# Kernel optimization log

Measured on AMD Instinct MI355X. Metric: run time of the kernel, lower is better.

## Reference

```python
import jax, jax.numpy as jnp
import numpy as np

# static architecture constants (match init_kwargs)
H, D, N_BASIS, MEM_LEN, QLEN = 16, 128, 1024, 512, 2048
RIDGE = 0.5
BASIS_SIGMAS = (0.005, 0.01)


def _gaussian_pdf(x, mu, sigma):
    return jnp.exp(-0.5 * ((x - mu) / sigma) ** 2) / (sigma * jnp.sqrt(2.0 * jnp.pi))


def _basis_params(n):
    # torch.meshgrid(linspace(0,1,n//2), sigmas, indexing='ij') then flatten
    m = jnp.linspace(0.0, 1.0, n // len(BASIS_SIGMAS)).astype(jnp.float32)
    mu = jnp.repeat(m, len(BASIS_SIGMAS))
    sigma = jnp.tile(jnp.asarray(BASIS_SIGMAS, jnp.float32), n // len(BASIS_SIGMAS))
    return mu, sigma


def _compute_G(l, b_mu, b_sigma, n):
    # padded linear positions on [-0.5+shift, 1.5-shift], l even -> 2l points
    shift = 1.0 / (2 * l)
    pos = jnp.linspace(-0.5 + shift, 1.5 - shift, 2 * l).astype(jnp.float32)
    F = _gaussian_pdf(pos[None, :], b_mu[:, None], b_sigma[:, None])  # [N, 2l]
    # G = F^T (F F^T + ridge I)^{-1}, then crop padding rows -> [l, N]
    G = jnp.linalg.solve(F @ F.T + RIDGE * jnp.eye(n, dtype=jnp.float32), F).T
    return G[l // 2: -(l // 2)]


def _forward(k, q, W_key, W_val, W_out, w_mu, w_sigma):
    d = H * D
    b_mu, b_sigma = _basis_params(N_BASIS)
    k = k[:, -512:, :]                                   # forward truncates memory
    l = k.shape[1]
    G = _compute_G(l, b_mu, b_sigma, N_BASIS)            # [l, N]
    # value_function: project signal onto basis coefficients B -> [1, N, d]
    B = jnp.einsum('bld,ln->bnd', k, G)
    keys = (B @ W_key.T).reshape(1, N_BASIS, H, D).transpose(0, 2, 1, 3)    # [1,H,N,D]
    values = (B @ W_val.T).reshape(1, N_BASIS, H, D).transpose(0, 2, 1, 3)  # [1,H,N,D]
    scores = jnp.einsum('bhqd,bhnd->bhqn', q / jnp.sqrt(jnp.float32(D)), keys)
    mu = jax.nn.sigmoid(scores @ w_mu)[..., None]                           # [1,H,Q,1]
    sigma_sq = jnp.maximum(jax.nn.softplus(scores @ w_sigma), 1e-4)[..., None]
    # continuous softmax over Gaussian RBFs: r_j = E_{t~N(mu,sigma_sq)}[psi_j(t)]
    # closed form: N(mu; b_mu_j, sigma_sq + b_sigma_j^2)
    r = _gaussian_pdf(b_mu, mu, jnp.sqrt(sigma_sq + b_sigma ** 2))          # [1,H,Q,N]
    context = jnp.einsum('bhqn,bhnd->bqhd', r, values).reshape(1, QLEN, d)
    return context @ W_out.T


def setup_inputs() -> dict:
    key = jax.random.key(0)
    ks = jax.random.split(key, 7)
    d = H * D
    s = 0.02
    return {
        'k': jax.random.normal(ks[0], (1, MEM_LEN, d), jnp.float32),
        'q': jax.random.normal(ks[1], (1, H, QLEN, D), jnp.float32),
        'W_key': jax.random.normal(ks[2], (d, d), jnp.float32) * s,
        'W_val': jax.random.normal(ks[3], (d, d), jnp.float32) * s,
        'W_out': jax.random.normal(ks[4], (d, d), jnp.float32) * s,
        'w_mu': jax.random.normal(ks[5], (N_BASIS,), jnp.float32) * s,
        'w_sigma': jax.random.normal(ks[6], (N_BASIS,), jnp.float32) * s,
        'new_doc': 1,
    }


def reference(k, q, W_key, W_val, W_out, w_mu, w_sigma, new_doc):
    # new_doc=True -> B_past/x_past reset, so only the fresh-memory path runs
    return _forward(k, q, W_key, W_val, W_out, w_mu, w_sigma)
```

## Files before the change

### kernel.cpp

```cpp
#include <hip/hip_runtime.h>
#include <hip/hip_bf16.h>
#include <vector>
#include <cmath>
#include <cstring>

using bf16 = __hip_bfloat16;
typedef short s16x8 __attribute__((ext_vector_type(8)));
typedef float f32x4 __attribute__((ext_vector_type(4)));

static constexpr int kH = 16, kD = 128, kNB = 1024, kML = 512, kQL = 2048, kDM = 2048;

static void compute_Gt_host(float* Gt) {
  const int n = kNB, P = 2 * kML;
  std::vector<double> F((size_t)n * P), A((size_t)n * n), pos(P);
  const double shift = 1.0 / (double)P;
  const double p0 = -0.5 + shift, p1 = 1.5 - shift;
  for (int i = 0; i < P; i++) pos[i] = p0 + (p1 - p0) * (double)i / (double)(P - 1);
  const double c0 = 0.3989422804014327;
  std::vector<int> lo(n), hi(n);
  for (int b = 0; b < n; b++) {
    double mu = (double)(b >> 1) / 511.0;
    double sg = (b & 1) ? 0.01 : 0.005;
    double c = c0 / sg;
    double* Fb = &F[(size_t)b * P];
    for (int i = 0; i < P; i++) { double t = (pos[i] - mu) / sg; Fb[i] = c * exp(-0.5 * t * t); }
    int l = 0; while (l < P - 1 && pos[l] < mu - 14.0 * sg) l++;
    int h = P - 1; while (h > 0 && pos[h] > mu + 14.0 * sg) h--;
    lo[b] = l; hi[b] = h;
  }
  for (int i = 0; i < n; i++) {
    const double* fi = &F[(size_t)i * P];
    for (int j = 0; j <= i; j++) {
      const double* fj = &F[(size_t)j * P];
      int a = lo[i] > lo[j] ? lo[i] : lo[j];
      int b2 = hi[i] < hi[j] ? hi[i] : hi[j];
      double s = 0.0;
      for (int k2 = a; k2 <= b2; k2++) s += fi[k2] * fj[k2];
      A[(size_t)i * n + j] = s;
      if (i != j) A[(size_t)j * n + i] = s;
    }
    A[(size_t)i * n + i] += 0.5;
  }
  for (int j = 0; j < n; j++) {
    double* Aj = &A[(size_t)j * n];
    double d = Aj[j];
    for (int k2 = 0; k2 < j; k2++) d -= Aj[k2] * Aj[k2];
    d = std::sqrt(d); Aj[j] = d;
    double inv = 1.0 / d;
    for (int i = j + 1; i < n; i++) {
      double* Ai = &A[(size_t)i * n];
      double s = Ai[j];
      for (int k2 = 0; k2 < j; k2++) s -= Ai[k2] * Aj[k2];
      Ai[j] = s * inv;
    }
  }
  for (int i = 0; i < n; i++) {
    double* yi = &F[(size_t)i * P];
    const double* Ai = &A[(size_t)i * n];
    for (int k2 = 0; k2 < i; k2++) {
      double lik = Ai[k2];
      const double* yk = &F[(size_t)k2 * P];
      for (int t = 0; t < P; t++) yi[t] -= lik * yk[t];
    }
    double inv = 1.0 / Ai[i];
    for (int t = 0; t < P; t++) yi[t] *= inv;
  }
  for (int i = n - 1; i >= 0; i--) {
    double* xi = &F[(size_t)i * P];
    for (int k2 = i + 1; k2 < n; k2++) {
      double lki = A[(size_t)k2 * n + i];
      const double* xk = &F[(size_t)k2 * P];
      for (int t = 0; t < P; t++) xi[t] -= lki * xk[t];
    }
    double inv = 1.0 / A[(size_t)i * n + i];
    for (int t = 0; t < P; t++) xi[t] *= inv;
  }
  for (int b = 0; b < n; b++)
    for (int l = 0; l < kML; l++)
      Gt[(size_t)b * kML + l] = (float)F[(size_t)b * P + (kML / 2) + l];
}

static unsigned short f2bf_host(float x) {
  unsigned u; std::memcpy(&u, &x, 4);
  unsigned r = (u + 0x7FFFu + ((u >> 16) & 1u)) >> 16;
  return (unsigned short)r;
}
static float bf2f_host(unsigned short b) {
  unsigned u = ((unsigned)b) << 16; float f; std::memcpy(&f, &u, 4); return f;
}

namespace {
struct Init {
  float* d_GtTf = nullptr;
  unsigned short* d_Gth = nullptr;
  unsigned short* d_Gtl = nullptr;
  float* h_GtTf_pinned = nullptr;
  unsigned short* h_Gth_pinned = nullptr;
  unsigned short* h_Gtl_pinned = nullptr;
  std::vector<float> h_GtTf;
  std::vector<unsigned short> h_Gth, h_Gtl;
  Init() {
    std::vector<float> h_Gt((size_t)kNB * kML);
    compute_Gt_host(h_Gt.data());
    h_GtTf.resize(h_Gt.size());
    h_Gth.resize(h_Gt.size());
    h_Gtl.resize(h_Gt.size());
    for (int n = 0; n < kNB; n++)
      for (int l = 0; l < kML; l++) {
        float v = h_Gt[(size_t)n * kML + l];
        h_GtTf[(size_t)l * kNB + n] = v;
        unsigned short hb = f2bf_host(v);
        h_Gth[(size_t)n * kML + l] = hb;
        h_Gtl[(size_t)n * kML + l] = f2bf_host(v - bf2f_host(hb));
      }
    const size_t fb = h_Gt.size() * 4, bb = h_Gt.size() * 2;
    if (hipMalloc((void**)&d_GtTf, fb) == hipSuccess) {
      if (hipMemcpy(d_GtTf, h_GtTf.data(), fb, hipMemcpyHostToDevice) != hipSuccess) { hipFree(d_GtTf); d_GtTf = nullptr; }
    }
    if (hipMalloc((void**)&d_Gth, bb) == hipSuccess) {
      if (hipMemcpy(d_Gth, h_Gth.data(), bb, hipMemcpyHostToDevice) != hipSuccess) { hipFree(d_Gth); d_Gth = nullptr; }
    }
    if (hipMalloc((void**)&d_Gtl, bb) == hipSuccess) {
      if (hipMemcpy(d_Gtl, h_Gtl.data(), bb, hipMemcpyHostToDevice) != hipSuccess) { hipFree(d_Gtl); d_Gtl = nullptr; }
    }
    if (!d_GtTf && hipHostMalloc((void**)&h_GtTf_pinned, fb, 0) == hipSuccess)
      std::memcpy(h_GtTf_pinned, h_GtTf.data(), fb);
    if (!d_Gth && hipHostMalloc((void**)&h_Gth_pinned, bb, 0) == hipSuccess)
      std::memcpy(h_Gth_pinned, h_Gth.data(), bb);
    if (!d_Gtl && hipHostMalloc((void**)&h_Gtl_pinned, bb, 0) == hipSuccess)
      std::memcpy(h_Gtl_pinned, h_Gtl.data(), bb);
  }
};
Init g_init;
}

__device__ inline short f2bf(float x) {
  unsigned u = __float_as_uint(x);
  unsigned r = (u + 0x7FFFu + ((u >> 16) & 1u)) >> 16;
  return (short)r;
}
__device__ inline float bf2f(short b) {
  return __uint_as_float(((unsigned)(unsigned short)b) << 16);
}

__global__ __launch_bounds__(256) void detect_kernel(const unsigned short* __restrict__ q,
                                                     int* __restrict__ flag) {
  int t = threadIdx.x;
  int bad = 0;
  for (int i = t; i < 4096; i += 256) {
    int e = (q[i] >> 7) & 0xFF;
    if (e >= 0x98) bad = 1;
  }
  __shared__ int s[256];
  s[t] = bad; __syncthreads();
  for (int k2 = 128; k2 > 0; k2 >>= 1) { if (t < k2) s[t] |= s[t + k2]; __syncthreads(); }
  if (t == 0) *flag = s[0];
}

__global__ __launch_bounds__(256) void conv_bf16(const void* __restrict__ in,
                                                 short* __restrict__ out, int n4,
                                                 const int* __restrict__ flag) {
  int i = blockIdx.x * 256 + threadIdx.x;
  if (i >= n4) return;
  if (*flag) {
    float4 v = ((const float4*)in)[i];
    short4 o; o.x = f2bf(v.x); o.y = f2bf(v.y); o.z = f2bf(v.z); o.w = f2bf(v.w);
    ((short4*)out)[i] = o;
  } else {
    ((short4*)out)[i] = ((const short4*)in)[i];
  }
}

__global__ __launch_bounds__(256) void gw_kernel(const float* __restrict__ GtT,
                                                 const void* __restrict__ wmu,
                                                 const void* __restrict__ wsg,
                                                 float* __restrict__ gw,
                                                 const int* __restrict__ flag) {
  const bool f32 = (*flag != 0);
  const int l = blockIdx.x, t = threadIdx.x;
  const float* row = GtT + (long long)l * kNB;
  float a = 0.f, b = 0.f;
  for (int n = t; n < kNB; n += 256) {
    float g = row[n];
    float wm_ = f32 ? ((const float*)wmu)[n] : bf2f(((const short*)wmu)[n]);
    float ws_ = f32 ? ((const float*)wsg)[n] : bf2f(((const short*)wsg)[n]);
    a += g * wm_; b += g * ws_;
  }
  __shared__ float red[2][256];
  red[0][t] = a; red[1][t] = b;
  __syncthreads();
  for (int s = 128; s > 0; s >>= 1) {
    if (t < s) { red[0][t] += red[0][t + s]; red[1][t] += red[1][t + s]; }
    __syncthreads();
  }
  if (t == 0) { gw[l] = red[0][0]; gw[kML + l] = red[1][0]; }
}

__global__ __launch_bounds__(256) void bwk_kernel(const void* __restrict__ kin,
                                                  const float* __restrict__ gw,
                                                  float* __restrict__ bw,
                                                  const int* __restrict__ flag) {
  const bool f32 = (*flag != 0);
  int j = blockIdx.x * 256 + threadIdx.x;
  int l0 = blockIdx.y * 32;
  float a = 0.f, b = 0.f;
  for (int l = l0; l < l0 + 32; l++) {
    float kv = f32 ? ((const float*)kin)[(long long)l * kDM + j]
                   : bf2f(((const short*)kin)[(long long)l * kDM + j]);
    a += kv * gw[l]; b += kv * gw[kML + l];
  }
  atomicAdd(&bw[j], a);
  atomicAdd(&bw[kDM + j], b);
}

__global__ __launch_bounds__(256) void kw_kernel(const void* __restrict__ Wk,
                                                 const float* __restrict__ bw,
                                                 float* __restrict__ kw,
                                                 const int* __restrict__ flag) {
  const bool f32 = (*flag != 0);
  int i = blockIdx.x;
  float smu = 0.f, ssg = 0.f;
  if (f32) {
    const float* row = (const float*)Wk + (long long)i * kDM;
    for (int j = threadIdx.x; j < kDM; j += 256) { float w = row[j]; smu += w * bw[j]; ssg += w * bw[kDM + j]; }
  } else {
    const short* row = (const short*)Wk + (long long)i * kDM;
    for (int j = threadIdx.x; j < kDM; j += 256) { float w = bf2f(row[j]); smu += w * bw[j]; ssg += w * bw[kDM + j]; }
  }
  __shared__ float red[2][256];
  red[0][threadIdx.x] = smu; red[1][threadIdx.x] = ssg;
  __syncthreads();
  for (int s = 128; s > 0; s >>= 1) {
    if (threadIdx.x < (unsigned)s) {
      red[0][threadIdx.x] += red[0][threadIdx.x + s];
      red[1][threadIdx.x] += red[1][threadIdx.x + s];
    }
    __syncthreads();
  }
  if (threadIdx.x == 0) { kw[i] = red[0][0]; kw[kDM + i] = red[1][0]; }
}

__global__ __launch_bounds__(256) void musig_kernel(const void* __restrict__ q,
                                                    const float* __restrict__ kw,
                                                    float* __restrict__ mu,
                                                    float* __restrict__ sigsq,
                                                    const int* __restrict__ flag) {
  const bool f32 = (*flag != 0);
  int w = threadIdx.x >> 6, lane = threadIdx.x & 63;
  int idx = blockIdx.x * 4 + w;
  int h = idx >> 11;
  const float* kmu = kw + h * kD;
  const float* ksg = kw + kDM + h * kD;
  float q0, q1;
  if (f32) {
    const float* qrow = (const float*)q + (long long)idx * kD;
    q0 = qrow[lane]; q1 = qrow[lane + 64];
  } else {
    const short* qrow = (const short*)q + (long long)idx * kD;
    q0 = bf2f(qrow[lane]); q1 = bf2f(qrow[lane + 64]);
  }
  float a = q0 * kmu[lane] + q1 * kmu[lane + 64];
  float b = q0 * ksg[lane] + q1 * ksg[lane + 64];
  for (int s = 32; s > 0; s >>= 1) { a += __shfl_xor(a, s); b += __shfl_xor(b, s); }
  if (lane == 0) {
    const float inv_sqrt_d = 0.08838834764831845f;
    float zm = a * inv_sqrt_d, zs = b * inv_sqrt_d;
    mu[idx] = 1.f / (1.f + __expf(-zm));
    float sp = (zs > 20.f) ? zs : log1pf(__expf(zs));
    sigsq[idx] = fmaxf(sp, 1e-4f);
  }
}

template <int CSTORE>
__global__ __launch_bounds__(256) void mfma_gemm_bt(
    const short* __restrict__ A0, int lda, long long sA,
    const short* __restrict__ BT0, int ldb, long long sB,
    void* __restrict__ C0, int ldc, long long sC,
    int K, const int* __restrict__ flag) {
  __shared__ s16x8 lA[512];
  __shared__ s16x8 lB[512];
  const short* A = A0 + (long long)blockIdx.z * sA;
  const short* BT = BT0 + (long long)blockIdx.z * sB;
  const int t = threadIdx.x;
  const int wave = t >> 6, lane = t & 63;
  const int quad = lane >> 4, l16 = lane & 15;
  const int wm = wave >> 1, wn = wave & 1;
  const int m0 = blockIdx.y * 128, n0 = blockIdx.x * 128;
  const int r0 = t >> 2, kc = t & 3;
  f32x4 acc[4][4];
  const f32x4 z = {0.f, 0.f, 0.f, 0.f};
#pragma unroll
  for (int i = 0; i < 4; i++)
#pragma unroll
    for (int j = 0; j < 4; j++) acc[i][j] = z;
  for (int k0 = 0; k0 < K; k0 += 32) {
#pragma unroll
    for (int i = 0; i < 2; i++) {
      int m = r0 + i * 64;
      int cidx = (m >> 4) * 64 + kc * 16 + (m & 15);
      lA[cidx] = *(const s16x8*)(A + (long long)(m0 + m) * lda + k0 + kc * 8);
      lB[cidx] = *(const s16x8*)(BT + (long long)(n0 + m) * ldb + k0 + kc * 8);
    }
    __syncthreads();
    s16x8 af[4], bfr[4];
#pragma unroll
    for (int i = 0; i < 4; i++) af[i] = lA[(wm * 4 + i) * 64 + lane];
#pragma unroll
    for (int j = 0; j < 4; j++) bfr[j] = lB[(wn * 4 + j) * 64 + lane];
#pragma unroll
    for (int i = 0; i < 4; i++)
#pragma unroll
      for (int j = 0; j < 4; j++)
        acc[i][j] = __builtin_amdgcn_mfma_f32_16x16x32_bf16(af[i], bfr[j], acc[i][j], 0, 0, 0);
    __syncthreads();
  }
  if (CSTORE == 0) {
    short* Cp = (short*)C0 + (long long)blockIdx.z * sC;
#pragma unroll
    for (int i = 0; i < 4; i++)
#pragma unroll
      for (int j = 0; j < 4; j++) {
        int gn = n0 + (wn * 4 + j) * 16 + l16;
#pragma unroll
        for (int rg = 0; rg < 4; rg++) {
          int gm = m0 + (wm * 4 + i) * 16 + quad * 4 + rg;
          Cp[(long long)gm * ldc + gn] = f2bf(acc[i][j][rg]);
        }
      }
  } else if (CSTORE == 1) {
    short* Cp = (short*)C0 + (long long)blockIdx.z * sC;
#pragma unroll
    for (int i = 0; i < 4; i++)
#pragma unroll
      for (int j = 0; j < 4; j++) {
        int gn = n0 + (wn * 4 + j) * 16 + l16;
        int gm = m0 + (wm * 4 + i) * 16 + quad * 4;
        short4 p; p.x = f2bf(acc[i][j][0]); p.y = f2bf(acc[i][j][1]);
        p.z = f2bf(acc[i][j][2]); p.w = f2bf(acc[i][j][3]);
        *(short4*)(Cp + (long long)gn * ldc + gm) = p;
      }
  } else {
    if (*flag) {
      float* Cp = (float*)C0 + (long long)blockIdx.z * sC;
#pragma unroll
      for (int i = 0; i < 4; i++)
#pragma unroll
        for (int j = 0; j < 4; j++) {
          int gn = n0 + (wn * 4 + j) * 16 + l16;
#pragma unroll
          for (int rg = 0; rg < 4; rg++) {
            int gm = m0 + (wm * 4 + i) * 16 + quad * 4 + rg;
            Cp[(long long)gm * ldc + gn] = acc[i][j][rg];
          }
        }
    } else {
      short* Cp = (short*)C0 + (long long)blockIdx.z * sC;
#pragma unroll
      for (int i = 0; i < 4; i++)
#pragma unroll
        for (int j = 0; j < 4; j++) {
          int gn = n0 + (wn * 4 + j) * 16 + l16;
#pragma unroll
          for (int rg = 0; rg < 4; rg++) {
            int gm = m0 + (wm * 4 + i) * 16 + quad * 4 + rg;
            Cp[(long long)gm * ldc + gn] = f2bf(acc[i][j][rg]);
          }
        }
    }
  }
}

__global__ __launch_bounds__(256) void mfma_gemm_bt2(
    const short* __restrict__ A0, int lda,
    const short* __restrict__ BTh, const short* __restrict__ BTl, int ldb,
    short* __restrict__ Ch, short* __restrict__ Cl, int ldc, int K) {
  __shared__ s16x8 lA[512], lBh[512], lBl[512];
  const int t = threadIdx.x;
  const int wave = t >> 6, lane = t & 63;
  const int quad = lane >> 4, l16 = lane & 15;
  const int wm = wave >> 1, wn = wave & 1;
  const int m0 = blockIdx.y * 128, n0 = blockIdx.x * 128;
  const int r0 = t >> 2, kc = t & 3;
  f32x4 acc[4][4];
  const f32x4 z = {0.f, 0.f, 0.f, 0.f};
#pragma unroll
  for (int i = 0; i < 4; i++)
#pragma unroll
    for (int j = 0; j < 4; j++) acc[i][j] = z;
  for (int k0 = 0; k0 < K; k0 += 32) {
#pragma unroll
    for (int i = 0; i < 2; i++) {
      int m = r0 + i * 64;
      int cidx = (m >> 4) * 64 + kc * 16 + (m & 15);
      lA[cidx]  = *(const s16x8*)(A0 + (long long)(m0 + m) * lda + k0 + kc * 8);
      lBh[cidx] = *(const s16x8*)(BTh + (long long)(n0 + m) * ldb + k0 + kc * 8);
      lBl[cidx] = *(const s16x8*)(BTl + (long long)(n0 + m) * ldb + k0 + kc * 8);
    }
    __syncthreads();
    s16x8 af[4], bh[4], bl[4];
#pragma unroll
    for (int i = 0; i < 4; i++) af[i] = lA[(wm * 4 + i) * 64 + lane];
#pragma unroll
    for (int j = 0; j < 4; j++) {
      bh[j] = lBh[(wn * 4 + j) * 64 + lane];
      bl[j] = lBl[(wn * 4 + j) * 64 + lane];
    }
#pragma unroll
    for (int i = 0; i < 4; i++)
#pragma unroll
      for (int j = 0; j < 4; j++) {
        acc[i][j] = __builtin_amdgcn_mfma_f32_16x16x32_bf16(af[i], bh[j], acc[i][j], 0, 0, 0);
        acc[i][j] = __builtin_amdgcn_mfma_f32_16x16x32_bf16(af[i], bl[j], acc[i][j], 0, 0, 0);
      }
    __syncthreads();
  }
#pragma unroll
  for (int i = 0; i < 4; i++)
#pragma unroll
    for (int j = 0; j < 4; j++) {
      int gn = n0 + (wn * 4 + j) * 16 + l16;
#pragma unroll
      for (int rg = 0; rg < 4; rg++) {
        int gm = m0 + (wm * 4 + i) * 16 + quad * 4 + rg;
        float v = acc[i][j][rg];
        short hb = f2bf(v);
        Ch[(long long)gm * ldc + gn] = hb;
        Cl[(long long)gm * ldc + gn] = f2bf(v - bf2f(hb));
      }
    }
}

__global__ __launch_bounds__(256) void mfma_rv(
    const float* __restrict__ mu_all, const float* __restrict__ s2_all,
    const short* __restrict__ VTh, const short* __restrict__ VTl,
    short* __restrict__ ctx) {
  __shared__ s16x8 lAh[512], lAl[512], lBh[512], lBl[512];
  const int t = threadIdx.x;
  const int wave = t >> 6, lane = t & 63;
  const int quad = lane >> 4, l16 = lane & 15;
  const int wm = wave >> 1, wn = wave & 1;
  const int h = blockIdx.z;
  const int m0 = blockIdx.y * 128;
  const int r0 = t >> 2, kc = t & 3;
  const long long voff = (long long)h * kD * kNB;
  float muv[2], ivs[2][2], cof[2][2];
#pragma unroll
  for (int i = 0; i < 2; i++) {
    int row = h * kQL + m0 + r0 + i * 64;
    float m_ = mu_all[row], s2 = s2_all[row];
    ivs[i][0] = rsqrtf(s2 + 2.5e-5f);
    ivs[i][1] = rsqrtf(s2 + 1e-4f);
    cof[i][0] = 0.3989422804014327f * ivs[i][0];
    cof[i][1] = 0.3989422804014327f * ivs[i][1];
    muv[i] = m_;
  }
  f32x4 acc[4][4];
  const f32x4 z = {0.f, 0.f, 0.f, 0.f};
#pragma unroll
  for (int i = 0; i < 4; i++)
#pragma unroll
    for (int j = 0; j < 4; j++) acc[i][j] = z;
  for (int k0 = 0; k0 < kNB; k0 += 32) {
#pragma unroll
    for (int i = 0; i < 2; i++) {
      int m = r0 + i * 64;
      int cidx = (m >> 4) * 64 + kc * 16 + (m & 15);
      s16x8 hv, lv;
#pragma unroll
      for (int jj = 0; jj < 8; jj++) {
        int n = k0 + kc * 8 + jj;
        float bmu = (float)(n >> 1) * (1.f / 511.f);
        int p = jj & 1;
        float tt = (bmu - muv[i]) * ivs[i][p];
        float v = cof[i][p] * __expf(-0.5f * tt * tt);
        short hb = f2bf(v);
        hv[jj] = hb;
        lv[jj] = f2bf(v - bf2f(hb));
      }
      lAh[cidx] = hv;
      lAl[cidx] = lv;
      lBh[cidx] = *(const s16x8*)(VTh + voff + (long long)m * kNB + k0 + kc * 8);
      lBl[cidx] = *(const s16x8*)(VTl + voff + (long long)m * kNB + k0 + kc * 8);
    }
    __syncthreads();
    s16x8 ah[4], al[4], bh[4], bl[4];
#pragma unroll
    for (int i = 0; i < 4; i++) {
      ah[i] = lAh[(wm * 4 + i) * 64 + lane];
      al[i] = lAl[(wm * 4 + i) * 64 + lane];
    }
#pragma unroll
    for (int j = 0; j < 4; j++) {
      bh[j] = lBh[(wn * 4 + j) * 64 + lane];
      bl[j] = lBl[(wn * 4 + j) * 64 + lane];
    }
#pragma unroll
    for (int i = 0; i < 4; i++)
#pragma unroll
      for (int j = 0; j < 4; j++) {
        acc[i][j] = __builtin_amdgcn_mfma_f32_16x16x32_bf16(ah[i], bh[j], acc[i][j], 0, 0, 0);
        acc[i][j] = __builtin_amdgcn_mfma_f32_16x16x32_bf16(ah[i], bl[j], acc[i][j], 0, 0, 0);
        acc[i][j] = __builtin_amdgcn_mfma_f32_16x16x32_bf16(al[i], bh[j], acc[i][j], 0, 0, 0);
      }
    __syncthreads();
  }
  short* Cp = ctx + h * kD;
#pragma unroll
  for (int i = 0; i < 4; i++)
#pragma unroll
    for (int j = 0; j < 4; j++) {
      int gn = (wn * 4 + j) * 16 + l16;
#pragma unroll
      for (int rg = 0; rg < 4; rg++) {
        int gm = m0 + (wm * 4 + i) * 16 + quad * 4 + rg;
        Cp[(long long)gm * kDM + gn] = f2bf(acc[i][j][rg]);
      }
    }
}

extern "C" void kernel_launch(void* const* d_in, const int* in_sizes, int n_in,
                              void* d_out, int out_size, void* d_ws, size_t ws_size,
                              hipStream_t stream) {
  (void)in_sizes; (void)n_in; (void)out_size; (void)ws_size;
  const void* kmem = d_in[0];
  const void* q    = d_in[1];
  const void* Wk   = d_in[2];
  const void* Wv   = d_in[3];
  const void* Wo   = d_in[4];
  const void* wmu  = d_in[5];
  const void* wsg  = d_in[6];

  char* ws = (char*)d_ws;
  short* k_bf  = (short*)ws;
  short* kvT   = (short*)(ws + ((size_t)2 << 20));
  short* Wv_bf = (short*)(ws + ((size_t)4 << 20));
  short* Wo_bf = Wv_bf;
  short* VTh   = (short*)(ws + ((size_t)12 << 20));
  short* VTl   = (short*)(ws + ((size_t)16 << 20));
  short* ctx   = (short*)(ws + ((size_t)20 << 20));
  float* tail  = (float*)(ws + ((size_t)28 << 20));
  float* gw    = tail;
  float* bw    = gw + 2 * kML;
  float* kw    = bw + 2 * kDM;
  float* mu    = kw + 2 * kDM;
  float* sigsq = mu + kH * kQL;
  int*   flag  = (int*)(sigsq + kH * kQL);
  float* gtffall = (float*)(ws + ((size_t)28 << 20) + ((size_t)1 << 19));
  short* ghfall  = (short*)(ws + ((size_t)30 << 20) + ((size_t)1 << 19));
  short* glfall  = (short*)(ws + ((size_t)31 << 20) + ((size_t)1 << 19));

  const float* GtTf = g_init.d_GtTf;
  if (!GtTf) {
    const void* src = g_init.h_GtTf_pinned ? (const void*)g_init.h_GtTf_pinned
                                           : (const void*)g_init.h_GtTf.data();
    hipMemcpyAsync(gtffall, src, (size_t)kNB * kML * 4, hipMemcpyHostToDevice, stream);
    GtTf = gtffall;
  }
  const short* Gh = (const short*)g_init.d_Gth;
  if (!Gh) {
    const void* src = g_init.h_Gth_pinned ? (const void*)g_init.h_Gth_pinned
                                          : (const void*)g_init.h_Gth.data();
    hipMemcpyAsync(ghfall, src, (size_t)kNB * kML * 2, hipMemcpyHostToDevice, stream);
    Gh = ghfall;
  }
  const short* Gl = (const short*)g_init.d_Gtl;
  if (!Gl) {
    const void* src = g_init.h_Gtl_pinned ? (const void*)g_init.h_Gtl_pinned
                                          : (const void*)g_init.h_Gtl.data();
    hipMemcpyAsync(glfall, src, (size_t)kNB * kML * 2, hipMemcpyHostToDevice, stream);
    Gl = glfall;
  }

  detect_kernel<<<1, 256, 0, stream>>>((const unsigned short*)q, flag);

  conv_bf16<<<(kML * kDM / 4 + 255) / 256, 256, 0, stream>>>(kmem, k_bf, kML * kDM / 4, flag);
  conv_bf16<<<(kDM * kDM / 4 + 255) / 256, 256, 0, stream>>>(Wv, Wv_bf, kDM * kDM / 4, flag);

  gw_kernel<<<kML, 256, 0, stream>>>(GtTf, wmu, wsg, gw, flag);
  hipMemsetAsync(bw, 0, 2 * kDM * sizeof(float), stream);
  bwk_kernel<<<dim3(kDM / 256, kML / 32), 256, 0, stream>>>(kmem, gw, bw, flag);
  kw_kernel<<<kDM, 256, 0, stream>>>(Wk, bw, kw, flag);
  musig_kernel<<<kH * kQL / 4, 256, 0, stream>>>(q, kw, mu, sigsq, flag);

  mfma_gemm_bt<1><<<dim3(kDM / 128, kML / 128, 1), 256, 0, stream>>>(
      k_bf, kDM, 0, Wv_bf, kDM, 0, kvT, kML, 0, kDM, flag);

  conv_bf16<<<(kDM * kDM / 4 + 255) / 256, 256, 0, stream>>>(Wo, Wo_bf, kDM * kDM / 4, flag);

  mfma_gemm_bt2<<<dim3(kNB / 128, kDM / 128, 1), 256, 0, stream>>>(
      kvT, kML, Gh, Gl, kML, VTh, VTl, kNB, kML);

  mfma_rv<<<dim3(1, kQL / 128, kH), 256, 0, stream>>>(mu, sigsq, VTh, VTl, ctx);

  mfma_gemm_bt<2><<<dim3(kDM / 128, kQL / 128, 1), 256, 0, stream>>>(
      ctx, kDM, 0, Wo_bf, kDM, 0, d_out, kDM, 0, kDM, flag);
}
```

Measured before the change: 320.9 us.

## Split-K the k·Wv GEMM with a transposing reduction; use direct global-to-LDS loads

The k×Wv^T GEMM (512×2048, K=2048) used to launch only 64 blocks. It is now split four ways along K into fp32 partial buffers, and a separate kernel sums the partials and writes the transposed bf16 kvT. The aim is better occupancy of the many CUs. Separately, all MFMA GEMM tile loads now use global_load_lds to write straight into LDS, skipping the register round trip. The cost is extra fp32 partial traffic, one more launch, and a Pbuf that aliases the VTh/VTl workspace region. The LDS layout produced by the direct loads must match the old fragment layout.

Result: faster. 308.2 us (-3.9%).

```diff
diff --git a/kernel.cpp b/kernel.cpp
--- a/kernel.cpp
+++ b/kernel.cpp
@@ -143,6 +143,13 @@
   return __uint_as_float(((unsigned)(unsigned short)b) << 16);
 }
 
+__device__ inline void gload16(const void* g, void* l) {
+  __builtin_amdgcn_global_load_lds(
+      (__attribute__((address_space(1))) void*)(g),
+      (__attribute__((address_space(3))) void*)(l),
+      16, 0, 0);
+}
+
 __global__ __launch_bounds__(256) void detect_kernel(const unsigned short* __restrict__ q,
                                                      int* __restrict__ flag) {
   int t = threadIdx.x;
@@ -286,7 +293,7 @@
   const int quad = lane >> 4, l16 = lane & 15;
   const int wm = wave >> 1, wn = wave & 1;
   const int m0 = blockIdx.y * 128, n0 = blockIdx.x * 128;
-  const int r0 = t >> 2, kc = t & 3;
+  const int srow = lane & 15, skc = lane >> 4;
   f32x4 acc[4][4];
   const f32x4 z = {0.f, 0.f, 0.f, 0.f};
 #pragma unroll
@@ -296,10 +303,10 @@
   for (int k0 = 0; k0 < K; k0 += 32) {
 #pragma unroll
     for (int i = 0; i < 2; i++) {
-      int m = r0 + i * 64;
-      int cidx = (m >> 4) * 64 + kc * 16 + (m & 15);
-      lA[cidx] = *(const s16x8*)(A + (long long)(m0 + m) * lda + k0 + kc * 8);
-      lB[cidx] = *(const s16x8*)(BT + (long long)(n0 + m) * ldb + k0 + kc * 8);
+      int sub = wave + i * 4;
+      int m = sub * 16 + srow;
+      gload16(A + (long long)(m0 + m) * lda + k0 + skc * 8, &lA[sub * 64]);
+      gload16(BT + (long long)(n0 + m) * ldb + k0 + skc * 8, &lB[sub * 64]);
     }
     __syncthreads();
     s16x8 af[4], bfr[4];
@@ -326,18 +333,6 @@
           int gm = m0 + (wm * 4 + i) * 16 + quad * 4 + rg;
           Cp[(long long)gm * ldc + gn] = f2bf(acc[i][j][rg]);
         }
-      }
-  } else if (CSTORE == 1) {
-    short* Cp = (short*)C0 + (long long)blockIdx.z * sC;
-#pragma unroll
-    for (int i = 0; i < 4; i++)
-#pragma unroll
-      for (int j = 0; j < 4; j++) {
-        int gn = n0 + (wn * 4 + j) * 16 + l16;
-        int gm = m0 + (wm * 4 + i) * 16 + quad * 4;
-        short4 p; p.x = f2bf(acc[i][j][0]); p.y = f2bf(acc[i][j][1]);
-        p.z = f2bf(acc[i][j][2]); p.w = f2bf(acc[i][j][3]);
-        *(short4*)(Cp + (long long)gn * ldc + gm) = p;
       }
   } else {
     if (*flag) {
@@ -367,6 +362,78 @@
           }
         }
     }
+  }
+}
+
+__global__ __launch_bounds__(256) void mfma_gemm_sk(
+    const short* __restrict__ A0, int lda,
+    const short* __restrict__ BT0, int ldb,
+    float* __restrict__ P, int ldc) {
+  __shared__ s16x8 lA[512], lB[512];
+  const int t = threadIdx.x;
+  const int wave = t >> 6, lane = t & 63;
+  const int quad = lane >> 4, l16 = lane & 15;
+  const int wm = wave >> 1, wn = wave & 1;
+  const int m0 = blockIdx.y * 128, n0 = blockIdx.x * 128;
+  const int kbeg = blockIdx.z * 512, kend = kbeg + 512;
+  const int srow = lane & 15, skc = lane >> 4;
+  f32x4 acc[4][4];
+  const f32x4 z = {0.f, 0.f, 0.f, 0.f};
+#pragma unroll
+  for (int i = 0; i < 4; i++)
+#pragma unroll
+    for (int j = 0; j < 4; j++) acc[i][j] = z;
+  for (int k0 = kbeg; k0 < kend; k0 += 32) {
+#pragma unroll
+    for (int i = 0; i < 2; i++) {
+      int sub = wave + i * 4;
+      int m = sub * 16 + srow;
+      gload16(A0 + (long long)(m0 + m) * lda + k0 + skc * 8, &lA[sub * 64]);
+      gload16(BT0 + (long long)(n0 + m) * ldb + k0 + skc * 8, &lB[sub * 64]);
+    }
+    __syncthreads();
+    s16x8 af[4], bfr[4];
+#pragma unroll
+    for (int i = 0; i < 4; i++) af[i] = lA[(wm * 4 + i) * 64 + lane];
+#pragma unroll
+    for (int j = 0; j < 4; j++) bfr[j] = lB[(wn * 4 + j) * 64 + lane];
+#pragma unroll
+    for (int i = 0; i < 4; i++)
+#pragma unroll
+      for (int j = 0; j < 4; j++)
+        acc[i][j] = __builtin_amdgcn_mfma_f32_16x16x32_bf16(af[i], bfr[j], acc[i][j], 0, 0, 0);
+    __syncthreads();
+  }
+  float* Cp = P + (long long)blockIdx.z * kML * kDM;
+#pragma unroll
+  for (int i = 0; i < 4; i++)
+#pragma unroll
+    for (int j = 0; j < 4; j++) {
+      int gn = n0 + (wn * 4 + j) * 16 + l16;
+#pragma unroll
+      for (int rg = 0; rg < 4; rg++) {
+        int gm = m0 + (wm * 4 + i) * 16 + quad * 4 + rg;
+        Cp[(long long)gm * ldc + gn] = acc[i][j][rg];
+      }
+    }
+}
+
+__global__ __launch_bounds__(256) void reduceT_kernel(const float* __restrict__ P,
+                                                      short* __restrict__ kvT) {
+  __shared__ float tile[64][65];
+  const int bd = blockIdx.x, bl = blockIdx.y;
+  const int tx = threadIdx.x & 63, ty = threadIdx.x >> 6;
+  for (int i = ty; i < 64; i += 4) {
+    int l = bl * 64 + i, d = bd * 64 + tx;
+    float s = 0.f;
+#pragma unroll
+    for (int z = 0; z < 4; z++) s += P[((long long)z * kML + l) * kDM + d];
+    tile[i][tx] = s;
+  }
+  __syncthreads();
+  for (int i = ty; i < 64; i += 4) {
+    int d = bd * 64 + i, l = bl * 64 + tx;
+    kvT[(long long)d * kML + l] = f2bf(tile[tx][i]);
   }
 }
 
@@ -380,7 +447,7 @@
   const int quad = lane >> 4, l16 = lane & 15;
   const int wm = wave >> 1, wn = wave & 1;
   const int m0 = blockIdx.y * 128, n0 = blockIdx.x * 128;
-  const int r0 = t >> 2, kc = t & 3;
+  const int srow = lane & 15, skc = lane >> 4;
   f32x4 acc[4][4];
   const f32x4 z = {0.f, 0.f, 0.f, 0.f};
 #pragma unroll
@@ -390,11 +457,11 @@
   for (int k0 = 0; k0 < K; k0 += 32) {
 #pragma unroll
     for (int i = 0; i < 2; i++) {
-      int m = r0 + i * 64;
-      int cidx = (m >> 4) * 64 + kc * 16 + (m & 15);
-      lA[cidx]  = *(const s16x8*)(A0 + (long long)(m0 + m) * lda + k0 + kc * 8);
-      lBh[cidx] = *(const s16x8*)(BTh + (long long)(n0 + m) * ldb + k0 + kc * 8);
-      lBl[cidx] = *(const s16x8*)(BTl + (long long)(n0 + m) * ldb + k0 + kc * 8);
+      int sub = wave + i * 4;
+      int m = sub * 16 + srow;
+      gload16(A0 + (long long)(m0 + m) * lda + k0 + skc * 8, &lA[sub * 64]);
+      gload16(BTh + (long long)(n0 + m) * ldb + k0 + skc * 8, &lBh[sub * 64]);
+      gload16(BTl + (long long)(n0 + m) * ldb + k0 + skc * 8, &lBl[sub * 64]);
     }
     __syncthreads();
     s16x8 af[4], bh[4], bl[4];
@@ -442,6 +509,7 @@
   const int h = blockIdx.z;
   const int m0 = blockIdx.y * 128;
   const int r0 = t >> 2, kc = t & 3;
+  const int srow = lane & 15, skc = lane >> 4;
   const long long voff = (long long)h * kD * kNB;
   float muv[2], ivs[2][2], cof[2][2];
 #pragma unroll
@@ -461,6 +529,13 @@
 #pragma unroll
     for (int j = 0; j < 4; j++) acc[i][j] = z;
   for (int k0 = 0; k0 < kNB; k0 += 32) {
+#pragma unroll
+    for (int i = 0; i < 2; i++) {
+      int sub = wave + i * 4;
+      int m = sub * 16 + srow;
+      gload16(VTh + voff + (long long)m * kNB + k0 + skc * 8, &lBh[sub * 64]);
+      gload16(VTl + voff + (long long)m * kNB + k0 + skc * 8, &lBl[sub * 64]);
+    }
 #pragma unroll
     for (int i = 0; i < 2; i++) {
       int m = r0 + i * 64;
@@ -479,8 +554,6 @@
       }
       lAh[cidx] = hv;
       lAl[cidx] = lv;
-      lBh[cidx] = *(const s16x8*)(VTh + voff + (long long)m * kNB + k0 + kc * 8);
-      lBl[cidx] = *(const s16x8*)(VTl + voff + (long long)m * kNB + k0 + kc * 8);
     }
     __syncthreads();
     s16x8 ah[4], al[4], bh[4], bl[4];
@@ -535,6 +608,7 @@
   short* kvT   = (short*)(ws + ((size_t)2 << 20));
   short* Wv_bf = (short*)(ws + ((size_t)4 << 20));
   short* Wo_bf = Wv_bf;
+  float* Pbuf  = (float*)(ws + ((size_t)12 << 20));
   short* VTh   = (short*)(ws + ((size_t)12 << 20));
   short* VTl   = (short*)(ws + ((size_t)16 << 20));
   short* ctx   = (short*)(ws + ((size_t)20 << 20));
@@ -582,8 +656,9 @@
   kw_kernel<<<kDM, 256, 0, stream>>>(Wk, bw, kw, flag);
   musig_kernel<<<kH * kQL / 4, 256, 0, stream>>>(q, kw, mu, sigsq, flag);
 
-  mfma_gemm_bt<1><<<dim3(kDM / 128, kML / 128, 1), 256, 0, stream>>>(
-      k_bf, kDM, 0, Wv_bf, kDM, 0, kvT, kML, 0, kDM, flag);
+  mfma_gemm_sk<<<dim3(kDM / 128, kML / 128, 4), 256, 0, stream>>>(
+      k_bf, kDM, Wv_bf, kDM, Pbuf, kDM);
+  reduceT_kernel<<<dim3(kDM / 64, kML / 64), 256, 0, stream>>>(Pbuf, kvT);
 
   conv_bf16<<<(kDM * kDM / 4 + 255) / 256, 256, 0, stream>>>(Wo, Wo_bf, kDM * kDM / 4, flag);
 
```
